# Optimization experiments

Hardware: AMD Instinct MI355X
Metric: run time of the kernel (lower is better)

Reference implementation:

```python
import jax, jax.numpy as jnp
import numpy as np
import math

IN_DIM = 2048
OUT_DIM = 2048
BATCH = 4096
BN_EPS = 1e-5


def setup_inputs() -> dict:
    key = jax.random.key(0)
    ks = jax.random.split(key, 6)
    x = jax.random.normal(ks[0], (BATCH, IN_DIM), dtype=jnp.float32)
    # scale ~ N(1.0, 0.1), translate = 0
    scale = 1.0 + 0.1 * jax.random.normal(ks[1], (1, IN_DIM), dtype=jnp.float32)
    translate = jnp.zeros((1, IN_DIM), dtype=jnp.float32)
    # kaiming-normal-ish init for wave_weight (fan_in), orthogonal-ish for base_weight
    wave_weight = jax.random.normal(ks[2], (OUT_DIM, IN_DIM), dtype=jnp.float32) * np.sqrt(2.0 / IN_DIM)
    bw = jax.random.normal(ks[3], (OUT_DIM, IN_DIM), dtype=jnp.float32)
    q, _ = jnp.linalg.qr(bw.T)  # (IN_DIM, OUT_DIM) orthonormal columns
    base_weight = q.T.astype(jnp.float32)
    gamma = jnp.ones((OUT_DIM,), dtype=jnp.float32)
    beta = jnp.zeros((OUT_DIM,), dtype=jnp.float32)
    return {"x": x, "scale": scale, "translate": translate,
            "wave_weight": wave_weight, "base_weight": base_weight,
            "gamma": gamma, "beta": beta}


def reference(x, scale, translate, wave_weight, base_weight, gamma, beta):
    # Bio wavelet: pi^-1/4 * cos(3u) * exp(-0.5 u^2), u = (x - t) / clamp(s, 1e-3)
    u = (x - translate) / jnp.maximum(scale, 1e-3)            # (B, in)
    wavelet = (math.pi ** -0.25) * jnp.cos(3.0 * u) * jnp.exp(-0.5 * u * u)
    # einsum 'boi,oi->bo' with singleton o broadcast == plain matmul
    wave_out = jnp.einsum('bi,oi->bo', wavelet, wave_weight)  # (B, out)
    base_out = jnp.einsum('bi,oi->bo', x, base_weight)        # (B, out)
    y = wave_out + 0.3 * base_out
    # BatchNorm1d (training mode: batch statistics, biased variance)
    mean = jnp.mean(y, axis=0)
    var = jnp.mean(jnp.square(y - mean), axis=0)
    out = gamma * (y - mean) * jax.lax.rsqrt(var + BN_EPS) + beta
    # dropout treated as identity (deterministic reference)
    return out
```

## Files before the change

kernel.cpp:

```cpp
#include <hip/hip_runtime.h>
#include <stdint.h>

#define IN_DIM 2048
#define OUT_DIM 2048
#define BATCH 4096
#define KDIM (2 * IN_DIM)
#define KROWB (KDIM * 2)
#define NT 64
#define BN_EPS 1e-5f

typedef __attribute__((ext_vector_type(8))) short bf16x8;
typedef __attribute__((ext_vector_type(4))) float f32x4;

__device__ __forceinline__ unsigned short f2bf(float f) {
  union { float f; unsigned u; } v; v.f = f;
  unsigned r = v.u + 0x7FFFu + ((v.u >> 16) & 1u);
  return (unsigned short)(r >> 16);
}

__global__ void prep_act(const float* __restrict__ x,
                         const float* __restrict__ scale,
                         const float* __restrict__ translate,
                         unsigned short* __restrict__ A) {
  int e = (blockIdx.x * 256 + threadIdx.x) * 4;
  int b = e / IN_DIM;
  int i = e % IN_DIM;
  float4 xv = *(const float4*)(x + e);
  float4 sv = *(const float4*)(scale + i);
  float4 tv = *(const float4*)(translate + i);
  const float c = 0.7511255444649425f;
  float u0 = (xv.x - tv.x) / fmaxf(sv.x, 1e-3f);
  float u1 = (xv.y - tv.y) / fmaxf(sv.y, 1e-3f);
  float u2 = (xv.z - tv.z) / fmaxf(sv.z, 1e-3f);
  float u3 = (xv.w - tv.w) / fmaxf(sv.w, 1e-3f);
  ushort4 wv, xb;
  wv.x = f2bf(c * __cosf(3.0f * u0) * __expf(-0.5f * u0 * u0));
  wv.y = f2bf(c * __cosf(3.0f * u1) * __expf(-0.5f * u1 * u1));
  wv.z = f2bf(c * __cosf(3.0f * u2) * __expf(-0.5f * u2 * u2));
  wv.w = f2bf(c * __cosf(3.0f * u3) * __expf(-0.5f * u3 * u3));
  xb.x = f2bf(xv.x); xb.y = f2bf(xv.y); xb.z = f2bf(xv.z); xb.w = f2bf(xv.w);
  *(ushort4*)(A + (size_t)b * KDIM + i) = wv;
  *(ushort4*)(A + (size_t)b * KDIM + IN_DIM + i) = xb;
}

__global__ void prep_w(const float* __restrict__ ww,
                       const float* __restrict__ bw,
                       unsigned short* __restrict__ W) {
  int e = (blockIdx.x * 256 + threadIdx.x) * 4;
  int o = e / IN_DIM;
  int k = e % IN_DIM;
  float4 a = *(const float4*)(ww + e);
  float4 b = *(const float4*)(bw + e);
  ushort4 wa, wb;
  wa.x = f2bf(a.x); wa.y = f2bf(a.y); wa.z = f2bf(a.z); wa.w = f2bf(a.w);
  wb.x = f2bf(0.3f * b.x); wb.y = f2bf(0.3f * b.y);
  wb.z = f2bf(0.3f * b.z); wb.w = f2bf(0.3f * b.w);
  *(ushort4*)(W + (size_t)o * KDIM + k) = wa;
  *(ushort4*)(W + (size_t)o * KDIM + IN_DIM + k) = wb;
}


#define GLDS(gp, lo) __builtin_amdgcn_global_load_lds( \
    (const __attribute__((address_space(1))) void*)(gp), \
    (__attribute__((address_space(3))) void*)(lds + (lo) + ldsl), 16, 0, 0)

#define STAGE(base_, gptr_, t_) do { \
  GLDS((gptr_) + (size_t)(t_) * 128, (base_)); \
  GLDS((gptr_) + (size_t)(t_) * 128 + (size_t)64 * KROWB, (base_) + 8192); \
} while (0)

#define LDA(dst, P, mh) do { \
  dst[0][0] = *(const bf16x8*)(lds + (P) + rA + (mh) * 4096 +    0 + s0); \
  dst[0][1] = *(const bf16x8*)(lds + (P) + rA + (mh) * 4096 +    0 + s1); \
  dst[1][0] = *(const bf16x8*)(lds + (P) + rA + (mh) * 4096 + 2048 + s0); \
  dst[1][1] = *(const bf16x8*)(lds + (P) + rA + (mh) * 4096 + 2048 + s1); \
} while (0)

#define LDB(dst, P, nh) do { \
  dst[0][0] = *(const bf16x8*)(lds + (P) + bu + rB + (nh) * 4096 +    0 + s0); \
  dst[0][1] = *(const bf16x8*)(lds + (P) + bu + rB + (nh) * 4096 +    0 + s1); \
  dst[1][0] = *(const bf16x8*)(lds + (P) + bu + rB + (nh) * 4096 + 2048 + s0); \
  dst[1][1] = *(const bf16x8*)(lds + (P) + bu + rB + (nh) * 4096 + 2048 + s1); \
} while (0)

#define MMQ(iof, jof, af, bf_) do { \
  __builtin_amdgcn_s_setprio(1); \
  _Pragma("unroll") for (int i2 = 0; i2 < 2; ++i2) \
  _Pragma("unroll") for (int j2 = 0; j2 < 2; ++j2) \
  _Pragma("unroll") for (int k2 = 0; k2 < 2; ++k2) \
    acc[(iof) + i2][(jof) + j2] = __builtin_amdgcn_mfma_f32_16x16x32_bf16( \
        af[i2][k2], bf_[j2][k2], acc[(iof) + i2][(jof) + j2], 0, 0, 0); \
  __builtin_amdgcn_s_setprio(0); \
} while (0)

#define LGKM0() asm volatile("s_waitcnt lgkmcnt(0)" ::: "memory")
#define VMW6()  asm volatile("s_waitcnt vmcnt(6)" ::: "memory")
#define VMW0()  asm volatile("s_waitcnt vmcnt(0)" ::: "memory")
#define BAR()   do { asm volatile("" ::: "memory"); __builtin_amdgcn_s_barrier(); \
                     asm volatile("" ::: "memory"); } while (0)

#define KTILE(p, t, DOSTAGE, VMTAIL) do { \
  const int P = (p) * 49152; \
  LDA(a0, P, 0); LDB(b0f, P, 0); \
  BAR(); MMQ(0, 0, a0, b0f); LGKM0(); BAR(); \
  LDB(b1f, P, 1); \
  BAR(); MMQ(0, 2, a0, b1f); LGKM0(); BAR(); \
  LDA(a1, P, 1); \
  if (DOSTAGE) STAGE(P + 16384, bS0, (t) + 2); \
  BAR(); MMQ(2, 2, a1, b1f); LGKM0(); BAR(); \
  if (DOSTAGE) { STAGE(P + 32768, bS1, (t) + 2); STAGE(P, aS, (t) + 2); } \
  BAR(); MMQ(2, 0, a1, b0f); VMTAIL; BAR(); \
} while (0)

__global__ __launch_bounds__(512, 2) void gemm8p(
    const unsigned short* __restrict__ A,
    const unsigned short* __restrict__ W,
    float* __restrict__ Y) {
  __shared__ char lds[98304];
  const int tid = threadIdx.x;
  const int lane = tid & 63;
  const int wave = tid >> 6;
  const int wm = wave >> 2;
  const int wn = wave & 3;

  const int sw = ((blockIdx.x & 7) << 5) | (blockIdx.x >> 3);
  const int bcol = (sw >> 5) * 256;
  const int brow = (sw & 31) * 128;

  const int srow = wave * 8 + (lane >> 3);
  const int gc16 = (lane & 7) ^ (lane >> 3);
  const char* aS  = (const char*)A + (size_t)(brow + srow) * KROWB + gc16 * 16;
  const char* bS0 = (const char*)W + (size_t)(bcol + srow) * KROWB + gc16 * 16;
  const char* bS1 = bS0 + (size_t)128 * KROWB;
  const int ldsl = wave * 1024;

  const int rA = (wm * 64 + (lane & 15)) * 128;
  const int rB = ((wn & 1) * 64 + (lane & 15)) * 128;
  const int bu = 16384 + (wn >> 1) * 16384;
  const int s0 = (((lane >> 4)    ) ^ (lane & 7)) << 4;
  const int s1 = ((4 + (lane >> 4)) ^ (lane & 7)) << 4;

  f32x4 acc[4][4];
#pragma unroll
  for (int m = 0; m < 4; ++m)
#pragma unroll
    for (int n = 0; n < 4; ++n)
      acc[m][n] = (f32x4){0.f, 0.f, 0.f, 0.f};
  bf16x8 a0[2][2], a1[2][2], b0f[2][2], b1f[2][2];

  STAGE(16384, bS0, 0); STAGE(32768, bS1, 0); STAGE(0, aS, 0);
  STAGE(49152 + 16384, bS0, 1); STAGE(49152 + 32768, bS1, 1); STAGE(49152, aS, 1);
  VMW6(); BAR();

  for (int t = 0; t < NT - 2; t += 2) {
    KTILE(0, t, 1, VMW6());
    KTILE(1, t + 1, 1, VMW6());
  }
  KTILE(0, NT - 2, 0, VMW0());
  KTILE(1, NT - 1, 0, VMW0());

  const int r0 = brow + wm * 64 + (lane >> 4) * 4;
  const int c0 = bcol + wn * 64 + (lane & 15);
#pragma unroll
  for (int m = 0; m < 4; ++m)
#pragma unroll
    for (int n = 0; n < 4; ++n)
#pragma unroll
      for (int j = 0; j < 4; ++j)
        Y[(size_t)(r0 + m * 16 + j) * OUT_DIM + (c0 + n * 16)] = acc[m][n][j];
}

__global__ void colstats(const float* __restrict__ Y,
                         float* __restrict__ sums, float* __restrict__ sqs) {
  int col = (blockIdx.x & 7) * 256 + threadIdx.x;
  int r0 = (blockIdx.x >> 3) * 128;
  float s = 0.f, q = 0.f;
  for (int r = 0; r < 128; ++r) {
    float v = Y[(size_t)(r0 + r) * OUT_DIM + col];
    s += v;
    q += v * v;
  }
  atomicAdd(&sums[col], s);
  atomicAdd(&sqs[col], q);
}

__global__ void bnorm(float* __restrict__ Y,
                      const float* __restrict__ sums, const float* __restrict__ sqs,
                      const float* __restrict__ gamma, const float* __restrict__ beta) {
  int e = (blockIdx.x * 256 + threadIdx.x) * 4;
  int c = e % OUT_DIM;
  float4 y = *(float4*)(Y + e);
  float4 s = *(const float4*)(sums + c);
  float4 q = *(const float4*)(sqs + c);
  float4 g = *(const float4*)(gamma + c);
  float4 bb = *(const float4*)(beta + c);
  const float invB = 1.0f / (float)BATCH;
  float m0 = s.x * invB, m1 = s.y * invB, m2 = s.z * invB, m3 = s.w * invB;
  float i0 = rsqrtf(q.x * invB - m0 * m0 + BN_EPS);
  float i1 = rsqrtf(q.y * invB - m1 * m1 + BN_EPS);
  float i2 = rsqrtf(q.z * invB - m2 * m2 + BN_EPS);
  float i3 = rsqrtf(q.w * invB - m3 * m3 + BN_EPS);
  y.x = g.x * (y.x - m0) * i0 + bb.x;
  y.y = g.y * (y.y - m1) * i1 + bb.y;
  y.z = g.z * (y.z - m2) * i2 + bb.z;
  y.w = g.w * (y.w - m3) * i3 + bb.w;
  *(float4*)(Y + e) = y;
}

extern "C" void kernel_launch(void* const* d_in, const int* in_sizes, int n_in,
                              void* d_out, int out_size, void* d_ws, size_t ws_size,
                              hipStream_t stream) {
  const float* x         = (const float*)d_in[0];
  const float* scale     = (const float*)d_in[1];
  const float* translate = (const float*)d_in[2];
  const float* ww        = (const float*)d_in[3];
  const float* bw        = (const float*)d_in[4];
  const float* gamma     = (const float*)d_in[5];
  const float* beta      = (const float*)d_in[6];
  float* out = (float*)d_out;

  char* ws = (char*)d_ws;
  unsigned short* A = (unsigned short*)ws;
  unsigned short* W = (unsigned short*)(ws + 33554432);
  float* sums = (float*)(ws + 33554432 + 16777216);
  float* sqs = sums + OUT_DIM;

  hipMemsetAsync(sums, 0, 2 * OUT_DIM * sizeof(float), stream);
  prep_act<<<(BATCH * IN_DIM) / 1024, 256, 0, stream>>>(x, scale, translate, A);
  prep_w<<<(OUT_DIM * IN_DIM) / 1024, 256, 0, stream>>>(ww, bw, W);
  gemm8p<<<256, 512, 0, stream>>>(A, W, out);
  colstats<<<256, 256, 0, stream>>>(out, sums, sqs);
  bnorm<<<(BATCH * OUT_DIM) / 1024, 256, 0, stream>>>(out, sums, sqs, gamma, beta);
}
```

Before: 117.3 us.

## Switch GEMM to 256x256 tiles with split-K and fuse partial sum into colstats

The GEMM goes from 128x256 output tiles to 256x256 tiles, with K split into two halves so the grid keeps 256 blocks. Each K half writes its own fp32 partial buffer. The column-statistics kernel now adds the second partial into the output while it accumulates sums. The larger tile raises arithmetic intensity per LDS byte and the pipeline is restaged with 128KB of LDS. The cost is an extra 32MB partial write and read, and the larger LDS footprint may limit occupancy to one block per CU despite launch_bounds(512,2).

```diff
diff --git a/kernel.cpp b/kernel.cpp
--- a/kernel.cpp
+++ b/kernel.cpp
@@ -6,7 +6,8 @@
 #define BATCH 4096
 #define KDIM (2 * IN_DIM)
 #define KROWB (KDIM * 2)
-#define NT 64
+#define KH 2048
+#define NTT 32
 #define BN_EPS 1e-5f
 
 typedef __attribute__((ext_vector_type(8))) short bf16x8;
@@ -64,59 +65,62 @@
     (const __attribute__((address_space(1))) void*)(gp), \
     (__attribute__((address_space(3))) void*)(lds + (lo) + ldsl), 16, 0, 0)
 
-#define STAGE(base_, gptr_, t_) do { \
-  GLDS((gptr_) + (size_t)(t_) * 128, (base_)); \
-  GLDS((gptr_) + (size_t)(t_) * 128 + (size_t)64 * KROWB, (base_) + 8192); \
-} while (0)
-
-#define LDA(dst, P, mh) do { \
-  dst[0][0] = *(const bf16x8*)(lds + (P) + rA + (mh) * 4096 +    0 + s0); \
-  dst[0][1] = *(const bf16x8*)(lds + (P) + rA + (mh) * 4096 +    0 + s1); \
-  dst[1][0] = *(const bf16x8*)(lds + (P) + rA + (mh) * 4096 + 2048 + s0); \
-  dst[1][1] = *(const bf16x8*)(lds + (P) + rA + (mh) * 4096 + 2048 + s1); \
-} while (0)
-
-#define LDB(dst, P, nh) do { \
-  dst[0][0] = *(const bf16x8*)(lds + (P) + bu + rB + (nh) * 4096 +    0 + s0); \
-  dst[0][1] = *(const bf16x8*)(lds + (P) + bu + rB + (nh) * 4096 +    0 + s1); \
-  dst[1][0] = *(const bf16x8*)(lds + (P) + bu + rB + (nh) * 4096 + 2048 + s0); \
-  dst[1][1] = *(const bf16x8*)(lds + (P) + bu + rB + (nh) * 4096 + 2048 + s1); \
-} while (0)
-
-#define MMQ(iof, jof, af, bf_) do { \
+#define STG(u_, gp_, t_) do { \
+  GLDS((gp_) + (size_t)(t_) * 128, (u_)); \
+  GLDS((gp_) + (size_t)64 * KROWB + (size_t)(t_) * 128, (u_) + 8192); \
+} while (0)
+
+#define LDA4(mh, ss) do { \
+  af[0] = *(const bf16x8*)(lds + P + rA + ((mh) * 4 + 0) * 2048 + (ss)); \
+  af[1] = *(const bf16x8*)(lds + P + rA + ((mh) * 4 + 1) * 2048 + (ss)); \
+  af[2] = *(const bf16x8*)(lds + P + rA + ((mh) * 4 + 2) * 2048 + (ss)); \
+  af[3] = *(const bf16x8*)(lds + P + rA + ((mh) * 4 + 3) * 2048 + (ss)); \
+} while (0)
+
+#define LDB4(dst, ss) do { \
+  dst[0] = *(const bf16x8*)(lds + P + rB + 0 * 2048 + (ss)); \
+  dst[1] = *(const bf16x8*)(lds + P + rB + 1 * 2048 + (ss)); \
+  dst[2] = *(const bf16x8*)(lds + P + rB + 2 * 2048 + (ss)); \
+  dst[3] = *(const bf16x8*)(lds + P + rB + 3 * 2048 + (ss)); \
+} while (0)
+
+#define MM16(mh, bfr) do { \
   __builtin_amdgcn_s_setprio(1); \
-  _Pragma("unroll") for (int i2 = 0; i2 < 2; ++i2) \
-  _Pragma("unroll") for (int j2 = 0; j2 < 2; ++j2) \
-  _Pragma("unroll") for (int k2 = 0; k2 < 2; ++k2) \
-    acc[(iof) + i2][(jof) + j2] = __builtin_amdgcn_mfma_f32_16x16x32_bf16( \
-        af[i2][k2], bf_[j2][k2], acc[(iof) + i2][(jof) + j2], 0, 0, 0); \
+  _Pragma("unroll") for (int i2 = 0; i2 < 4; ++i2) \
+  _Pragma("unroll") for (int j2 = 0; j2 < 4; ++j2) \
+    acc[(mh) * 4 + i2][j2] = __builtin_amdgcn_mfma_f32_16x16x32_bf16( \
+        af[i2], bfr[j2], acc[(mh) * 4 + i2][j2], 0, 0, 0); \
   __builtin_amdgcn_s_setprio(0); \
 } while (0)
 
 #define LGKM0() asm volatile("s_waitcnt lgkmcnt(0)" ::: "memory")
-#define VMW6()  asm volatile("s_waitcnt vmcnt(6)" ::: "memory")
+#define VMW4()  asm volatile("s_waitcnt vmcnt(4)" ::: "memory")
 #define VMW0()  asm volatile("s_waitcnt vmcnt(0)" ::: "memory")
 #define BAR()   do { asm volatile("" ::: "memory"); __builtin_amdgcn_s_barrier(); \
                      asm volatile("" ::: "memory"); } while (0)
 
-#define KTILE(p, t, DOSTAGE, VMTAIL) do { \
-  const int P = (p) * 49152; \
-  LDA(a0, P, 0); LDB(b0f, P, 0); \
-  BAR(); MMQ(0, 0, a0, b0f); LGKM0(); BAR(); \
-  LDB(b1f, P, 1); \
-  BAR(); MMQ(0, 2, a0, b1f); LGKM0(); BAR(); \
-  LDA(a1, P, 1); \
-  if (DOSTAGE) STAGE(P + 16384, bS0, (t) + 2); \
-  BAR(); MMQ(2, 2, a1, b1f); LGKM0(); BAR(); \
-  if (DOSTAGE) { STAGE(P + 32768, bS1, (t) + 2); STAGE(P, aS, (t) + 2); } \
-  BAR(); MMQ(2, 0, a1, b0f); VMTAIL; BAR(); \
-} while (0)
-
-__global__ __launch_bounds__(512, 2) void gemm8p(
+#define KTILE(u, DOST, DOST2, TAILB) do { \
+  const int P = ((u) & 1) << 16; \
+  const int Q = P ^ 65536; \
+  LDA4(0, s0); LDB4(b0, s0); \
+  if (DOST) STG(Q + 49152, bS1, (u) + 1); \
+  BAR(); MM16(0, b0); LGKM0(); VMW4(); BAR(); \
+  LDA4(1, s0); \
+  if (DOST) STG(Q + 0, aS0, (u) + 1); \
+  BAR(); MM16(1, b0); LGKM0(); BAR(); \
+  LDA4(0, s1); LDB4(b1, s1); \
+  if (DOST) STG(Q + 16384, aS1, (u) + 1); \
+  BAR(); MM16(0, b1); LGKM0(); BAR(); \
+  LDA4(1, s1); \
+  if (DOST2) STG(P + 32768, bS0, (u) + 2); \
+  BAR(); MM16(1, b1); LGKM0(); TAILB; BAR(); \
+} while (0)
+
+__global__ __launch_bounds__(512, 2) void gemm256(
     const unsigned short* __restrict__ A,
     const unsigned short* __restrict__ W,
-    float* __restrict__ Y) {
-  __shared__ char lds[98304];
+    float* __restrict__ P0, float* __restrict__ P1) {
+  __shared__ char lds[131072];
   const int tid = threadIdx.x;
   const int lane = tid & 63;
   const int wave = tid >> 6;
@@ -124,59 +128,63 @@
   const int wn = wave & 3;
 
   const int sw = ((blockIdx.x & 7) << 5) | (blockIdx.x >> 3);
-  const int bcol = (sw >> 5) * 256;
-  const int brow = (sw & 31) * 128;
-
-  const int srow = wave * 8 + (lane >> 3);
-  const int gc16 = (lane & 7) ^ (lane >> 3);
-  const char* aS  = (const char*)A + (size_t)(brow + srow) * KROWB + gc16 * 16;
-  const char* bS0 = (const char*)W + (size_t)(bcol + srow) * KROWB + gc16 * 16;
+  const int kz = sw >> 7;
+  const int brow = ((sw >> 3) & 15) * 256;
+  const int bcol = (sw & 7) * 256;
+  const size_t kb = (size_t)kz * (KH * 2);
+
+  const int srow = tid >> 3;
+  const int gc16 = (tid & 7) ^ (srow & 7);
+  const char* aS0 = (const char*)A + (size_t)(brow + srow) * KROWB + kb + gc16 * 16;
+  const char* aS1 = aS0 + (size_t)128 * KROWB;
+  const char* bS0 = (const char*)W + (size_t)(bcol + srow) * KROWB + kb + gc16 * 16;
   const char* bS1 = bS0 + (size_t)128 * KROWB;
   const int ldsl = wave * 1024;
 
-  const int rA = (wm * 64 + (lane & 15)) * 128;
-  const int rB = ((wn & 1) * 64 + (lane & 15)) * 128;
-  const int bu = 16384 + (wn >> 1) * 16384;
+  const int rA = (wm * 128 + (lane & 15)) * 128;
+  const int rB = 32768 + (wn * 64 + (lane & 15)) * 128;
   const int s0 = (((lane >> 4)    ) ^ (lane & 7)) << 4;
   const int s1 = ((4 + (lane >> 4)) ^ (lane & 7)) << 4;
 
-  f32x4 acc[4][4];
-#pragma unroll
-  for (int m = 0; m < 4; ++m)
+  f32x4 acc[8][4];
+#pragma unroll
+  for (int m = 0; m < 8; ++m)
 #pragma unroll
     for (int n = 0; n < 4; ++n)
       acc[m][n] = (f32x4){0.f, 0.f, 0.f, 0.f};
-  bf16x8 a0[2][2], a1[2][2], b0f[2][2], b1f[2][2];
-
-  STAGE(16384, bS0, 0); STAGE(32768, bS1, 0); STAGE(0, aS, 0);
-  STAGE(49152 + 16384, bS0, 1); STAGE(49152 + 32768, bS1, 1); STAGE(49152, aS, 1);
-  VMW6(); BAR();
-
-  for (int t = 0; t < NT - 2; t += 2) {
-    KTILE(0, t, 1, VMW6());
-    KTILE(1, t + 1, 1, VMW6());
-  }
-  KTILE(0, NT - 2, 0, VMW0());
-  KTILE(1, NT - 1, 0, VMW0());
-
-  const int r0 = brow + wm * 64 + (lane >> 4) * 4;
+  bf16x8 af[4], b0[4], b1[4];
+
+  STG(32768, bS0, 0); STG(49152, bS1, 0); STG(0, aS0, 0); STG(16384, aS1, 0);
+  STG(65536 + 32768, bS0, 1);
+  VMW4(); BAR();
+
+  for (int u = 0; u < NTT - 2; ++u)
+    KTILE(u, 1, 1, VMW4());
+  KTILE(NTT - 2, 1, 0, VMW0());
+  KTILE(NTT - 1, 0, 0, VMW0());
+
+  float* Pz = kz ? P1 : P0;
+  const int r0 = brow + wm * 128 + (lane >> 4) * 4;
   const int c0 = bcol + wn * 64 + (lane & 15);
 #pragma unroll
-  for (int m = 0; m < 4; ++m)
+  for (int m = 0; m < 8; ++m)
 #pragma unroll
     for (int n = 0; n < 4; ++n)
 #pragma unroll
       for (int j = 0; j < 4; ++j)
-        Y[(size_t)(r0 + m * 16 + j) * OUT_DIM + (c0 + n * 16)] = acc[m][n][j];
-}
-
-__global__ void colstats(const float* __restrict__ Y,
-                         float* __restrict__ sums, float* __restrict__ sqs) {
+        Pz[(size_t)(r0 + m * 16 + j) * OUT_DIM + (c0 + n * 16)] = acc[m][n][j];
+}
+
+__global__ void colstats2(const float* __restrict__ P1,
+                          float* __restrict__ Y,
+                          float* __restrict__ sums, float* __restrict__ sqs) {
   int col = (blockIdx.x & 7) * 256 + threadIdx.x;
   int r0 = (blockIdx.x >> 3) * 128;
   float s = 0.f, q = 0.f;
   for (int r = 0; r < 128; ++r) {
-    float v = Y[(size_t)(r0 + r) * OUT_DIM + col];
+    size_t idx = (size_t)(r0 + r) * OUT_DIM + col;
+    float v = Y[idx] + P1[idx];
+    Y[idx] = v;
     s += v;
     q += v * v;
   }
@@ -222,13 +230,14 @@
   char* ws = (char*)d_ws;
   unsigned short* A = (unsigned short*)ws;
   unsigned short* W = (unsigned short*)(ws + 33554432);
-  float* sums = (float*)(ws + 33554432 + 16777216);
-  float* sqs = sums + OUT_DIM;
+  float* P1   = (float*)(ws + 50331648);
+  float* sums = (float*)(ws + 83886080);
+  float* sqs  = sums + OUT_DIM;
 
   hipMemsetAsync(sums, 0, 2 * OUT_DIM * sizeof(float), stream);
   prep_act<<<(BATCH * IN_DIM) / 1024, 256, 0, stream>>>(x, scale, translate, A);
   prep_w<<<(OUT_DIM * IN_DIM) / 1024, 256, 0, stream>>>(ww, bw, W);
-  gemm8p<<<256, 512, 0, stream>>>(A, W, out);
-  colstats<<<256, 256, 0, stream>>>(out, sums, sqs);
+  gemm256<<<256, 512, 0, stream>>>(A, W, out, P1);
+  colstats2<<<256, 256, 0, stream>>>(P1, out, sums, sqs);
   bnorm<<<(BATCH * OUT_DIM) / 1024, 256, 0, stream>>>(out, sums, sqs, gamma, beta);
 }
```

Result: slower. 122.5 us (+4.5%).
